# Kernel optimization log

Measured on AMD Instinct MI355X. Metric: run time of the kernel, lower is better.

## Reference

```python
import jax, jax.numpy as jnp
import numpy as np

V, E, H = 50000, 256, 512
BS, SEQ = 64, 200


def setup_inputs() -> dict:
    key = jax.random.key(0)
    ks = jax.random.split(key, 16)
    s = 0.05
    return {
        "input_idx": jax.random.randint(ks[0], (BS,), 0, V),
        "encoded": jax.random.normal(ks[1], (BS, SEQ, 2 * H), jnp.float32),
        "encoded_idx": jax.random.randint(ks[2], (BS, SEQ), 0, V),
        "prev_state": jax.random.normal(ks[3], (BS, H), jnp.float32),
        "weighted": jax.random.normal(ks[4], (BS, 1, 2 * H), jnp.float32),
        "order": 1,
        "embed_W": jax.random.normal(ks[5], (V, E), jnp.float32) * s,
        "Wih": jax.random.normal(ks[6], (3 * H, E + 2 * H), jnp.float32) * s,
        "Whh": jax.random.normal(ks[7], (3 * H, H), jnp.float32) * s,
        "bih": jax.random.normal(ks[8], (3 * H,), jnp.float32) * s,
        "bhh": jax.random.normal(ks[9], (3 * H,), jnp.float32) * s,
        "Ws_W": jax.random.normal(ks[10], (H, 2 * H), jnp.float32) * s,
        "Ws_b": jax.random.normal(ks[11], (H,), jnp.float32) * s,
        "Wo_W": jax.random.normal(ks[12], (V, H), jnp.float32) * s,
        "Wo_b": jax.random.normal(ks[13], (V,), jnp.float32) * s,
        "Wc_W": jax.random.normal(ks[14], (H, 2 * H), jnp.float32) * s,
        "Wc_b": jax.random.normal(ks[15], (H,), jnp.float32) * s,
    }


def reference(input_idx, encoded, encoded_idx, prev_state, weighted, order,
              embed_W, Wih, Whh, bih, bhh, Ws_W, Ws_b, Wo_W, Wo_b, Wc_W, Wc_b):
    bs, seq, _ = encoded.shape
    hidden = Ws_W.shape[0]
    vocab = Wo_W.shape[0]

    if order == 0:
        prev_state = encoded[:, 1] @ Ws_W.T + Ws_b            # [bs, H]
        weighted = jnp.zeros((bs, 1, 2 * hidden), encoded.dtype)

    # GRU single step (batch_first, seq len 1)
    x = jnp.concatenate([embed_W[input_idx], weighted[:, 0, :]], axis=1)  # [bs, E+2H]
    gi = x @ Wih.T + bih                                       # [bs, 3H]
    gh = prev_state @ Whh.T + bhh                              # [bs, 3H]
    i_r, i_z, i_n = jnp.split(gi, 3, axis=1)
    h_r, h_z, h_n = jnp.split(gh, 3, axis=1)
    r = jax.nn.sigmoid(i_r + h_r)
    z = jax.nn.sigmoid(i_z + h_z)
    n = jnp.tanh(i_n + r * h_n)
    state = (1.0 - z) * n + z * prev_state                     # [bs, H]

    # generate and copy scores
    score_g = state @ Wo_W.T + Wo_b                            # [bs, V]
    sc = jnp.tanh(encoded @ Wc_W.T + Wc_b)                     # [bs, seq, H]
    score_c = jnp.einsum('bsh,bh->bs', sc, state)              # [bs, seq]
    enc_mask = jnp.where(encoded_idx == 0, -1000.0, 0.0).astype(score_c.dtype)
    score_c = jnp.tanh(score_c + enc_mask)

    probs = jax.nn.softmax(jnp.concatenate([score_g, score_c], axis=1), axis=1)
    prob_g = probs[:, :vocab]                                  # [bs, V]
    prob_c = probs[:, vocab:]                                  # [bs, seq]

    # scatter-add copy probs into vocab slots
    prob_c_to_g = jnp.zeros((bs, vocab), probs.dtype).at[
        jnp.arange(bs)[:, None], encoded_idx].add(prob_c)
    out = (prob_g + prob_c_to_g)[:, None, :]                   # [bs, 1, V]

    # selective-read attention over positions matching input token
    m = (encoded_idx == input_idx[:, None]).astype(encoded.dtype)  # [bs, seq]
    ssum = m.sum(axis=1, keepdims=True)
    m = jnp.where(ssum > 1, m / ssum, m)
    attn = (prob_c * m)[:, None, :]                            # [bs, 1, seq]
    weighted_out = attn @ encoded                              # [bs, 1, 2H]

    return out, state, weighted_out
```

## Files before the change

### kernel.cpp

```cpp
#include <hip/hip_runtime.h>

#define V 50000
#define E_DIM 256
#define H_DIM 512
#define H2 1024
#define G3 1536
#define BSZ 64
#define SEQ 200
#define KX 1280
#define MROWS 12800
#define NBLK_WO 782

#define XBF_OFF   0
#define H0_OFF    40960
#define H0BF_OFF  73728
#define GI_OFF    90112
#define GH_OFF    188416
#define STBF_OFF  286720
#define WCBF_OFF  303104
#define SC_OFF    565248
#define REDG_OFF  616448
#define RED_OFF   716544
#define ENCBF_OFF 716672

#define OUT_STATE 3200000
#define OUT_W     3232768

typedef __attribute__((ext_vector_type(8))) short bf16x8;
typedef __attribute__((ext_vector_type(4))) float f32x4;

__device__ __forceinline__ float sigmf(float x) { return 1.f / (1.f + __expf(-x)); }

__device__ __forceinline__ ushort f2bf(float f) {
  uint u = __float_as_uint(f);
  uint r = (u + 0x7FFFu + ((u >> 16) & 1u)) >> 16;
  return (ushort)r;
}

__device__ __forceinline__ float tanhfast(float x) {
  float xc = fminf(15.f, fmaxf(-15.f, x));
  float e = __expf(2.f * xc);
  return (e - 1.f) * __builtin_amdgcn_rcpf(e + 1.f);
}

__device__ __forceinline__ bf16x8 cvt8(float4 a, float4 b) {
  union { bf16x8 v; uint u[4]; } r;
  asm("v_cvt_pk_bf16_f32 %0, %1, %2" : "=v"(r.u[0]) : "v"(a.x), "v"(a.y));
  asm("v_cvt_pk_bf16_f32 %0, %1, %2" : "=v"(r.u[1]) : "v"(a.z), "v"(a.w));
  asm("v_cvt_pk_bf16_f32 %0, %1, %2" : "=v"(r.u[2]) : "v"(b.x), "v"(b.y));
  asm("v_cvt_pk_bf16_f32 %0, %1, %2" : "=v"(r.u[3]) : "v"(b.z), "v"(b.w));
  return r.v;
}

__device__ __forceinline__ void gload16(const void* g, void* l) {
  __builtin_amdgcn_global_load_lds(
      (__attribute__((address_space(1))) void*)(g),
      (__attribute__((address_space(3))) void*)(l), 16, 0, 0);
}

__global__ void kprep(const float* __restrict__ Wc_W, ushort* __restrict__ Wc_bf,
                      const float* __restrict__ encoded, ushort* __restrict__ enc_bf,
                      const int* __restrict__ input_idx,
                      const float* __restrict__ prev_state, const float* __restrict__ weighted,
                      const int* __restrict__ order_p, const float* __restrict__ embed_W,
                      const float* __restrict__ Ws_W, const float* __restrict__ Ws_b,
                      ushort* __restrict__ x_bf, float* __restrict__ h0,
                      ushort* __restrict__ h0_bf) {
  int bid = blockIdx.x, tid = threadIdx.x;
  if (bid < 512) {
    int i = bid * 256 + tid;
    float4 v = ((const float4*)Wc_W)[i];
    ushort4 o;
    o.x = f2bf(v.x); o.y = f2bf(v.y); o.z = f2bf(v.z); o.w = f2bf(v.w);
    ((ushort4*)Wc_bf)[i] = o;
    return;
  }
  if (bid < 3712) {
    int base = (bid - 512) * 1024;
#pragma unroll
    for (int j = 0; j < 4; ++j) {
      int i = base + j * 256 + tid;
      float4 v = ((const float4*)encoded)[i];
      ushort4 o;
      o.x = f2bf(v.x); o.y = f2bf(v.y); o.z = f2bf(v.z); o.w = f2bf(v.w);
      ((ushort4*)enc_bf)[i] = o;
    }
    return;
  }
  int b = bid - 3712;
  int order = order_p[0];
  int idx = input_idx[b];
  x_bf[b * KX + tid] = f2bf(embed_W[(size_t)idx * E_DIM + tid]);
  if (order != 0) {
    for (int j = tid; j < H2; j += 256) x_bf[b * KX + E_DIM + j] = f2bf(weighted[b * H2 + j]);
    for (int j = tid; j < H_DIM; j += 256) {
      float v = prev_state[b * H_DIM + j];
      h0[b * H_DIM + j] = v;
      h0_bf[b * H_DIM + j] = f2bf(v);
    }
  } else {
    for (int j = tid; j < H2; j += 256) x_bf[b * KX + E_DIM + j] = 0;
    const float* er = encoded + ((size_t)b * SEQ + 1) * H2;
    for (int j = tid; j < H_DIM; j += 256) {
      float acc = Ws_b[j];
      const float* wr = Ws_W + (size_t)j * H2;
      for (int k = 0; k < H2; ++k) acc = fmaf(er[k], wr[k], acc);
      h0[b * H_DIM + j] = acc;
      h0_bf[b * H_DIM + j] = f2bf(acc);
    }
  }
}

__device__ __forceinline__ void gemm_small(const ushort* __restrict__ Abf,
                                           const float* __restrict__ W,
                                           const float* __restrict__ bias,
                                           float* __restrict__ out, int N, int kdim,
                                           int bid) {
  int tid = threadIdx.x;
  int lane = tid & 63, wv = tid >> 6;
  int l15 = lane & 15, lg = lane >> 4;
  int n0 = (bid * 4 + wv) * 16;
  int col = n0 + l15;
  bool valid = col < N;
  int colc = valid ? col : N - 1;
  f32x4 acc[4];
#pragma unroll
  for (int mt = 0; mt < 4; ++mt) acc[mt] = (f32x4){0.f, 0.f, 0.f, 0.f};
  const float* wrow = W + (size_t)colc * kdim + lg * 8;
  const ushort* arow = Abf + (size_t)l15 * kdim + lg * 8;
#pragma unroll 4
  for (int k0 = 0; k0 < kdim; k0 += 32) {
    float4 w0 = *(const float4*)(wrow + k0);
    float4 w1 = *(const float4*)(wrow + k0 + 4);
    bf16x8 bf = cvt8(w0, w1);
#pragma unroll
    for (int mt = 0; mt < 4; ++mt) {
      bf16x8 af = *(const bf16x8*)(arow + (size_t)mt * 16 * kdim + k0);
      acc[mt] = __builtin_amdgcn_mfma_f32_16x16x32_bf16(af, bf, acc[mt], 0, 0, 0);
    }
  }
  float bv = bias[colc];
  if (valid) {
#pragma unroll
    for (int mt = 0; mt < 4; ++mt)
#pragma unroll
      for (int r = 0; r < 4; ++r)
        out[(size_t)(mt * 16 + lg * 4 + r) * N + col] = acc[mt][r] + bv;
  }
}

__global__ __launch_bounds__(256) void mfma_gates(const ushort* __restrict__ x_bf,
                                                  const float* __restrict__ Wih,
                                                  const float* __restrict__ bih,
                                                  const ushort* __restrict__ h0_bf,
                                                  const float* __restrict__ Whh,
                                                  const float* __restrict__ bhh,
                                                  float* __restrict__ gi, float* __restrict__ gh) {
  if (blockIdx.y == 0)
    gemm_small(x_bf, Wih, bih, gi, G3, KX, blockIdx.x);
  else
    gemm_small(h0_bf, Whh, bhh, gh, G3, H_DIM, blockIdx.x);
}

__global__ void k2_gru(const float* __restrict__ gi, const float* __restrict__ gh,
                       const float* __restrict__ h0, float* __restrict__ state_out,
                       ushort* __restrict__ state_bf) {
  int b = blockIdx.x, j = threadIdx.x;
  float ir = gi[b * G3 + j], iz = gi[b * G3 + H_DIM + j], inn = gi[b * G3 + 2 * H_DIM + j];
  float hr = gh[b * G3 + j], hz = gh[b * G3 + H_DIM + j], hn = gh[b * G3 + 2 * H_DIM + j];
  float r = sigmf(ir + hr);
  float z = sigmf(iz + hz);
  float n = tanhf(inn + r * hn);
  float st = (1.f - z) * n + z * h0[b * H_DIM + j];
  state_out[b * H_DIM + j] = st;
  state_bf[b * H_DIM + j] = f2bf(st);
}

__global__ __launch_bounds__(256) void wo_stage(const ushort* __restrict__ state_bf,
                                                const float* __restrict__ Wo_W,
                                                const float* __restrict__ Wo_b,
                                                float* __restrict__ out,
                                                float* __restrict__ redg) {
  __shared__ char ldsW[4][4][2048];
  __shared__ float sm[4][64], ss[4][64];
  int tid = threadIdx.x, lane = tid & 63, wv = tid >> 6;
  int l15 = lane & 15, lg = lane >> 4;
  int bid = blockIdx.x;
  int col0 = bid * 64 + wv * 16 + l15;
  bool v0ok = col0 < V;
  int cc0 = v0ok ? col0 : V - 1;
  const float* s0 = Wo_W + (size_t)cc0 * H_DIM + lg * 8;
  const ushort* aptr = state_bf + (size_t)l15 * H_DIM + lg * 8;

  f32x4 acc[4];
#pragma unroll
  for (int mt = 0; mt < 4; ++mt) acc[mt] = (f32x4){0.f, 0.f, 0.f, 0.f};

#define STGW(buf, it) do {                      \
    char* d_ = &ldsW[wv][buf][0];               \
    gload16(s0 + (it) * 32,     d_);            \
    gload16(s0 + (it) * 32 + 4, d_ + 1024);     \
  } while (0)

  STGW(0, 0); STGW(1, 1); STGW(2, 2);
  asm volatile("" ::: "memory");
#pragma unroll 1
  for (int it = 0; it < 16; ++it) {
    int cur = it & 3;
    bf16x8 af0 = *(const bf16x8*)(aptr + 0 * 16 * H_DIM + it * 32);
    bf16x8 af1 = *(const bf16x8*)(aptr + 1 * 16 * H_DIM + it * 32);
    bf16x8 af2 = *(const bf16x8*)(aptr + 2 * 16 * H_DIM + it * 32);
    bf16x8 af3 = *(const bf16x8*)(aptr + 3 * 16 * H_DIM + it * 32);
    if (it == 0) {
      STGW(3, 3);
      asm volatile("s_waitcnt vmcnt(10)" ::: "memory");
    } else if (it == 1) {
      STGW(0, 4);
      asm volatile("s_waitcnt vmcnt(14)" ::: "memory");
    } else if (it < 13) {
      STGW((it + 3) & 3, it + 3);
      asm volatile("s_waitcnt vmcnt(18)" ::: "memory");
    } else if (it == 13) {
      asm volatile("s_waitcnt vmcnt(16)" ::: "memory");
    } else if (it == 14) {
      asm volatile("s_waitcnt vmcnt(14)" ::: "memory");
    } else {
      asm volatile("s_waitcnt vmcnt(12)" ::: "memory");
    }
    const char* base = &ldsW[wv][cur][0];
    float4 w00 = *(const float4*)(base + lane * 16);
    float4 w01 = *(const float4*)(base + 1024 + lane * 16);
    bf16x8 wf0 = cvt8(w00, w01);
    acc[0] = __builtin_amdgcn_mfma_f32_16x16x32_bf16(af0, wf0, acc[0], 0, 0, 0);
    acc[1] = __builtin_amdgcn_mfma_f32_16x16x32_bf16(af1, wf0, acc[1], 0, 0, 0);
    acc[2] = __builtin_amdgcn_mfma_f32_16x16x32_bf16(af2, wf0, acc[2], 0, 0, 0);
    acc[3] = __builtin_amdgcn_mfma_f32_16x16x32_bf16(af3, wf0, acc[3], 0, 0, 0);
  }
#undef STGW

  float bv0 = Wo_b[cc0];
#pragma unroll
  for (int mt = 0; mt < 4; ++mt)
#pragma unroll
    for (int r = 0; r < 4; ++r) {
      size_t row = (size_t)(mt * 16 + lg * 4 + r) * V;
      if (v0ok) out[row + col0] = acc[mt][r] + bv0;
    }
#pragma unroll
  for (int mt = 0; mt < 4; ++mt)
#pragma unroll
    for (int r = 0; r < 4; ++r) {
      float a0 = v0ok ? acc[mt][r] + bv0 : -1e30f;
      float mx = a0;
#pragma unroll
      for (int off = 1; off < 16; off <<= 1) mx = fmaxf(mx, __shfl_xor(mx, off, 64));
      float e = v0ok ? __expf(a0 - mx) : 0.f;
#pragma unroll
      for (int off = 1; off < 16; off <<= 1) e += __shfl_xor(e, off, 64);
      if (l15 == 0) {
        sm[wv][mt * 16 + lg * 4 + r] = mx;
        ss[wv][mt * 16 + lg * 4 + r] = e;
      }
    }
  __syncthreads();
  if (tid < 64) {
    float M = -1e30f, S = 0.f;
#pragma unroll
    for (int w = 0; w < 4; ++w) {
      float m2 = sm[w][tid], s2 = ss[w][tid];
      float mn = fmaxf(M, m2);
      S = S * __expf(M - mn) + s2 * __expf(m2 - mn);
      M = mn;
    }
    redg[((size_t)tid * NBLK_WO + bid) * 2] = M;
    redg[((size_t)tid * NBLK_WO + bid) * 2 + 1] = S;
  }
}

__global__ __launch_bounds__(256) void k4_mfma9(const ushort* __restrict__ enc_bf,
                                                const ushort* __restrict__ Wc_bf,
                                                const float* __restrict__ Wc_b,
                                                const float* __restrict__ state,
                                                float* __restrict__ scpart) {
  __shared__ char lds[2][24576];
  __shared__ float sred[4][64];
  int tid = threadIdx.x, lane = tid & 63, wv = tid >> 6;
  int l15 = lane & 15, lg = lane >> 4;
  int bid = blockIdx.x;
  int mtile = bid >> 2, ntile = bid & 3;
  int m0 = mtile * 64, n0 = ntile * 128;

  const ushort* asrc = enc_bf + (size_t)(m0 + wv * 16 + l15) * H2 + lg * 8;
  const ushort* bsrc0 = Wc_bf + (size_t)(n0 + (wv * 2 + 0) * 16 + l15) * H2 + lg * 8;
  const ushort* bsrc1 = Wc_bf + (size_t)(n0 + (wv * 2 + 1) * 16 + l15) * H2 + lg * 8;

  f32x4 acc[4][2];
#pragma unroll
  for (int mf = 0; mf < 4; ++mf)
#pragma unroll
    for (int nf = 0; nf < 2; ++nf) acc[mf][nf] = (f32x4){0.f, 0.f, 0.f, 0.f};

#define STG(buf, it) do {                                              \
    char* d_ = &lds[buf][0];                                           \
    gload16(asrc + (it) * 64,       d_ + (wv * 2 + 0) * 1024);         \
    gload16(asrc + (it) * 64 + 32,  d_ + (wv * 2 + 1) * 1024);         \
    gload16(bsrc0 + (it) * 64,      d_ + 8192 + (wv * 4 + 0) * 1024);  \
    gload16(bsrc0 + (it) * 64 + 32, d_ + 8192 + (wv * 4 + 1) * 1024);  \
    gload16(bsrc1 + (it) * 64,      d_ + 8192 + (wv * 4 + 2) * 1024);  \
    gload16(bsrc1 + (it) * 64 + 32, d_ + 8192 + (wv * 4 + 3) * 1024);  \
  } while (0)

  STG(0, 0);
  __syncthreads();
#pragma unroll 1
  for (int it = 0; it < 16; ++it) {
    int cur = it & 1;
    if (it < 15) STG(cur ^ 1, it + 1);
    const char* base = &lds[cur][0];
#pragma unroll
    for (int ks = 0; ks < 2; ++ks) {
      bf16x8 b0 = *(const bf16x8*)(base + 8192 + (wv * 4 + ks) * 1024 + lane * 16);
      bf16x8 b1 = *(const bf16x8*)(base + 8192 + (wv * 4 + 2 + ks) * 1024 + lane * 16);
#pragma unroll
      for (int mf = 0; mf < 4; ++mf) {
        bf16x8 a = *(const bf16x8*)(base + (mf * 2 + ks) * 1024 + lane * 16);
        acc[mf][0] = __builtin_amdgcn_mfma_f32_16x16x32_bf16(a, b0, acc[mf][0], 0, 0, 0);
        acc[mf][1] = __builtin_amdgcn_mfma_f32_16x16x32_bf16(a, b1, acc[mf][1], 0, 0, 0);
      }
    }
    __syncthreads();
  }
#undef STG

  float pv[4][4];
#pragma unroll
  for (int mf = 0; mf < 4; ++mf)
#pragma unroll
    for (int r = 0; r < 4; ++r) pv[mf][r] = 0.f;
#pragma unroll
  for (int nfl = 0; nfl < 2; ++nfl) {
    int n = n0 + (wv * 2 + nfl) * 16 + l15;
    float bias = Wc_b[n];
#pragma unroll
    for (int mf = 0; mf < 4; ++mf) {
      int mrow = m0 + mf * 16 + lg * 4;
#pragma unroll
      for (int r = 0; r < 4; ++r) {
        int b = (mrow + r) / SEQ;
        pv[mf][r] += tanhfast(acc[mf][nfl][r] + bias) * state[b * H_DIM + n];
      }
    }
  }
#pragma unroll
  for (int off = 1; off < 16; off <<= 1)
#pragma unroll
    for (int mf = 0; mf < 4; ++mf)
#pragma unroll
      for (int r = 0; r < 4; ++r) pv[mf][r] += __shfl_xor(pv[mf][r], off, 64);
  if (l15 == 0) {
#pragma unroll
    for (int mf = 0; mf < 4; ++mf)
#pragma unroll
      for (int r = 0; r < 4; ++r) sred[wv][mf * 16 + lg * 4 + r] = pv[mf][r];
  }
  __syncthreads();
  if (tid < 64) {
    float s = sred[0][tid] + sred[1][tid] + sred[2][tid] + sred[3][tid];
    scpart[(size_t)ntile * MROWS + m0 + tid] = s;
  }
}

__global__ void kred(const float* __restrict__ redg, const float* __restrict__ scpart,
                     const int* __restrict__ eidx, float* __restrict__ red) {
  int b = blockIdx.x, tid = threadIdx.x;
  float m = -1e30f, s = 0.f;
  for (int i = tid; i < NBLK_WO; i += 256) {
    float m2 = redg[((size_t)b * NBLK_WO + i) * 2];
    float s2 = redg[((size_t)b * NBLK_WO + i) * 2 + 1];
    float mn = fmaxf(m, m2);
    s = s * __expf(m - mn) + s2 * __expf(m2 - mn);
    m = mn;
  }
  for (int i = tid; i < SEQ; i += 256) {
    int idx = b * SEQ + i;
    int ei = eidx[idx];
    float scv = scpart[idx] + scpart[MROWS + idx] + scpart[2 * MROWS + idx] +
                scpart[3 * MROWS + idx];
    float sc = tanhf(scv + (ei == 0 ? -1000.f : 0.f));
    float mn = fmaxf(m, sc);
    s = s * __expf(m - mn) + __expf(sc - mn);
    m = mn;
  }
  __shared__ float ms[256], ssh[256];
  ms[tid] = m; ssh[tid] = s;
  __syncthreads();
  for (int off = 128; off > 0; off >>= 1) {
    if (tid < off) {
      float m2 = ms[tid + off], s2 = ssh[tid + off];
      float mn = fmaxf(ms[tid], m2);
      ssh[tid] = ssh[tid] * __expf(ms[tid] - mn) + s2 * __expf(m2 - mn);
      ms[tid] = mn;
    }
    __syncthreads();
  }
  if (tid == 0) {
    red[b * 2] = ms[0];
    red[b * 2 + 1] = ssh[0];
  }
}

__global__ void k7_probs(float* __restrict__ sg, const float* __restrict__ red) {
  int i = blockIdx.x * 256 + threadIdx.x;
  int b = i / 12500;
  float mm = red[b * 2], rd = 1.f / red[b * 2 + 1];
  float4* p = (float4*)sg;
  float4 v = p[i];
  v.x = __expf(v.x - mm) * rd;
  v.y = __expf(v.y - mm) * rd;
  v.z = __expf(v.z - mm) * rd;
  v.w = __expf(v.w - mm) * rd;
  p[i] = v;
}

__global__ void k8_copy(const float* __restrict__ scpart, const int* __restrict__ eidx,
                        const int* __restrict__ input_idx, const float* __restrict__ red,
                        const float* __restrict__ encoded, float* __restrict__ out,
                        float* __restrict__ wout) {
  int b = blockIdx.x, tid = threadIdx.x;
  __shared__ float att_s[SEQ];
  __shared__ int cnt_s[256];
  float mm = red[b * 2], rd = 1.f / red[b * 2 + 1];
  int inp = input_idx[b];
  int cnt = 0;
  for (int s = tid; s < SEQ; s += 256) {
    int idx = b * SEQ + s;
    int ei = eidx[idx];
    float scv = scpart[idx] + scpart[MROWS + idx] + scpart[2 * MROWS + idx] +
                scpart[3 * MROWS + idx];
    float sc = tanhf(scv + (ei == 0 ? -1000.f : 0.f));
    float p = __expf(sc - mm) * rd;
    bool mt = (ei == inp);
    att_s[s] = mt ? p : 0.f;
    cnt += mt ? 1 : 0;
    atomicAdd(&out[(size_t)b * V + ei], p);
  }
  cnt_s[tid] = cnt;
  __syncthreads();
  for (int off = 128; off > 0; off >>= 1) {
    if (tid < off) cnt_s[tid] += cnt_s[tid + off];
    __syncthreads();
  }
  int c = cnt_s[0];
  float scale = (c > 1) ? 1.f / (float)c : 1.f;
  float w0 = 0, w1 = 0, w2 = 0, w3 = 0;
  for (int s = 0; s < SEQ; ++s) {
    float a = att_s[s];
    if (a != 0.f) {
      const float* er = encoded + ((size_t)b * SEQ + s) * H2;
      w0 += a * er[tid];
      w1 += a * er[tid + 256];
      w2 += a * er[tid + 512];
      w3 += a * er[tid + 768];
    }
  }
  wout[b * H2 + tid] = w0 * scale;
  wout[b * H2 + tid + 256] = w1 * scale;
  wout[b * H2 + tid + 512] = w2 * scale;
  wout[b * H2 + tid + 768] = w3 * scale;
}

extern "C" void kernel_launch(void* const* d_in, const int* in_sizes, int n_in,
                              void* d_out, int out_size, void* d_ws, size_t ws_size,
                              hipStream_t stream) {
  const int* input_idx = (const int*)d_in[0];
  const float* encoded = (const float*)d_in[1];
  const int* encoded_idx = (const int*)d_in[2];
  const float* prev_state = (const float*)d_in[3];
  const float* weighted = (const float*)d_in[4];
  const int* order_p = (const int*)d_in[5];
  const float* embed_W = (const float*)d_in[6];
  const float* Wih = (const float*)d_in[7];
  const float* Whh = (const float*)d_in[8];
  const float* bih = (const float*)d_in[9];
  const float* bhh = (const float*)d_in[10];
  const float* Ws_W = (const float*)d_in[11];
  const float* Ws_b = (const float*)d_in[12];
  const float* Wo_W = (const float*)d_in[13];
  const float* Wo_b = (const float*)d_in[14];
  const float* Wc_W = (const float*)d_in[15];
  const float* Wc_b = (const float*)d_in[16];

  float* ws = (float*)d_ws;
  float* out = (float*)d_out;
  ushort* x_bf = (ushort*)(ws + XBF_OFF);
  float* h0 = ws + H0_OFF;
  ushort* h0_bf = (ushort*)(ws + H0BF_OFF);
  float* gi = ws + GI_OFF;
  float* gh = ws + GH_OFF;
  ushort* state_bf = (ushort*)(ws + STBF_OFF);
  ushort* Wc_bf = (ushort*)(ws + WCBF_OFF);
  float* scpart = ws + SC_OFF;
  float* redg = ws + REDG_OFF;
  float* red = ws + RED_OFF;
  ushort* enc_bf = (ushort*)(ws + ENCBF_OFF);
  float* state = out + OUT_STATE;
  float* wout = out + OUT_W;

  kprep<<<3776, 256, 0, stream>>>(Wc_W, Wc_bf, encoded, enc_bf, input_idx, prev_state,
                                  weighted, order_p, embed_W, Ws_W, Ws_b, x_bf, h0, h0_bf);
  mfma_gates<<<dim3(24, 2), 256, 0, stream>>>(x_bf, Wih, bih, h0_bf, Whh, bhh, gi, gh);
  k2_gru<<<64, 512, 0, stream>>>(gi, gh, h0, state, state_bf);
  wo_stage<<<NBLK_WO, 256, 0, stream>>>(state_bf, Wo_W, Wo_b, out, redg);
  k4_mfma9<<<800, 256, 0, stream>>>(enc_bf, Wc_bf, Wc_b, state, scpart);
  kred<<<64, 256, 0, stream>>>(redg, scpart, encoded_idx, red);
  k7_probs<<<3125, 256, 0, stream>>>(out, red);
  k8_copy<<<64, 256, 0, stream>>>(scpart, encoded_idx, input_idx, red, encoded, out, wout);
}
```

Measured before the change: 179.4 us.

## Split Wo projection across batch halves and stage state tile in LDS

Launches the output projection with a second grid dimension so each block handles 32 of the 64 batch rows, doubling the block count. The block's state rows are staged once into LDS instead of being re-read from global each iteration, and the weight prefetch shrinks from a 4-deep to a 2-deep buffer. Each Wo_W column tile, the dominant fp32 traffic, is now fetched by two blocks instead of one, in exchange for more parallelism and fewer accumulators per wave.

```diff
diff --git a/kernel.cpp b/kernel.cpp
--- a/kernel.cpp
+++ b/kernel.cpp
@@ -181,76 +181,69 @@
                                                 const float* __restrict__ Wo_b,
                                                 float* __restrict__ out,
                                                 float* __restrict__ redg) {
-  __shared__ char ldsW[4][4][2048];
-  __shared__ float sm[4][64], ss[4][64];
+  __shared__ char ldsA[32768];
+  __shared__ char ldsW[2][4][2048];
+  __shared__ float sm[4][32], ss[4][32];
   int tid = threadIdx.x, lane = tid & 63, wv = tid >> 6;
   int l15 = lane & 15, lg = lane >> 4;
-  int bid = blockIdx.x;
+  int bid = blockIdx.x, yh = blockIdx.y;
   int col0 = bid * 64 + wv * 16 + l15;
   bool v0ok = col0 < V;
   int cc0 = v0ok ? col0 : V - 1;
   const float* s0 = Wo_W + (size_t)cc0 * H_DIM + lg * 8;
-  const ushort* aptr = state_bf + (size_t)l15 * H_DIM + lg * 8;
-
-  f32x4 acc[4];
-#pragma unroll
-  for (int mt = 0; mt < 4; ++mt) acc[mt] = (f32x4){0.f, 0.f, 0.f, 0.f};
-
-#define STGW(buf, it) do {                      \
-    char* d_ = &ldsW[wv][buf][0];               \
-    gload16(s0 + (it) * 32,     d_);            \
-    gload16(s0 + (it) * 32 + 4, d_ + 1024);     \
-  } while (0)
-
-  STGW(0, 0); STGW(1, 1); STGW(2, 2);
-  asm volatile("" ::: "memory");
+
+#pragma unroll
+  for (int j = 0; j < 8; ++j) {
+    int slot = wv * 8 + j;
+    int mf = slot >> 4, it = slot & 15;
+    gload16(state_bf + (size_t)(yh * 32 + mf * 16 + l15) * H_DIM + it * 32 + lg * 8,
+            ldsA + slot * 1024);
+  }
+  {
+    char* d_ = &ldsW[0][wv][0];
+    gload16(s0, d_);
+    gload16(s0 + 4, d_ + 1024);
+  }
+  __syncthreads();
+
+  f32x4 acc[2];
+  acc[0] = (f32x4){0.f, 0.f, 0.f, 0.f};
+  acc[1] = (f32x4){0.f, 0.f, 0.f, 0.f};
+
 #pragma unroll 1
   for (int it = 0; it < 16; ++it) {
-    int cur = it & 3;
-    bf16x8 af0 = *(const bf16x8*)(aptr + 0 * 16 * H_DIM + it * 32);
-    bf16x8 af1 = *(const bf16x8*)(aptr + 1 * 16 * H_DIM + it * 32);
-    bf16x8 af2 = *(const bf16x8*)(aptr + 2 * 16 * H_DIM + it * 32);
-    bf16x8 af3 = *(const bf16x8*)(aptr + 3 * 16 * H_DIM + it * 32);
-    if (it == 0) {
-      STGW(3, 3);
-      asm volatile("s_waitcnt vmcnt(10)" ::: "memory");
-    } else if (it == 1) {
-      STGW(0, 4);
-      asm volatile("s_waitcnt vmcnt(14)" ::: "memory");
-    } else if (it < 13) {
-      STGW((it + 3) & 3, it + 3);
-      asm volatile("s_waitcnt vmcnt(18)" ::: "memory");
-    } else if (it == 13) {
-      asm volatile("s_waitcnt vmcnt(16)" ::: "memory");
-    } else if (it == 14) {
-      asm volatile("s_waitcnt vmcnt(14)" ::: "memory");
+    int cur = it & 1;
+    if (it < 15) {
+      char* d_ = &ldsW[cur ^ 1][wv][0];
+      gload16(s0 + (it + 1) * 32, d_);
+      gload16(s0 + (it + 1) * 32 + 4, d_ + 1024);
+      asm volatile("s_waitcnt vmcnt(2)" ::: "memory");
     } else {
-      asm volatile("s_waitcnt vmcnt(12)" ::: "memory");
-    }
-    const char* base = &ldsW[wv][cur][0];
-    float4 w00 = *(const float4*)(base + lane * 16);
-    float4 w01 = *(const float4*)(base + 1024 + lane * 16);
+      asm volatile("s_waitcnt vmcnt(0)" ::: "memory");
+    }
+    const char* wb = &ldsW[cur][wv][0];
+    float4 w00 = *(const float4*)(wb + lane * 16);
+    float4 w01 = *(const float4*)(wb + 1024 + lane * 16);
     bf16x8 wf0 = cvt8(w00, w01);
+    bf16x8 af0 = *(const bf16x8*)(ldsA + (0 * 16 + it) * 1024 + lane * 16);
+    bf16x8 af1 = *(const bf16x8*)(ldsA + (1 * 16 + it) * 1024 + lane * 16);
     acc[0] = __builtin_amdgcn_mfma_f32_16x16x32_bf16(af0, wf0, acc[0], 0, 0, 0);
     acc[1] = __builtin_amdgcn_mfma_f32_16x16x32_bf16(af1, wf0, acc[1], 0, 0, 0);
-    acc[2] = __builtin_amdgcn_mfma_f32_16x16x32_bf16(af2, wf0, acc[2], 0, 0, 0);
-    acc[3] = __builtin_amdgcn_mfma_f32_16x16x32_bf16(af3, wf0, acc[3], 0, 0, 0);
-  }
-#undef STGW
+  }
 
   float bv0 = Wo_b[cc0];
 #pragma unroll
-  for (int mt = 0; mt < 4; ++mt)
+  for (int mf = 0; mf < 2; ++mf)
 #pragma unroll
     for (int r = 0; r < 4; ++r) {
-      size_t row = (size_t)(mt * 16 + lg * 4 + r) * V;
-      if (v0ok) out[row + col0] = acc[mt][r] + bv0;
-    }
-#pragma unroll
-  for (int mt = 0; mt < 4; ++mt)
+      size_t row = (size_t)(yh * 32 + mf * 16 + lg * 4 + r) * V;
+      if (v0ok) out[row + col0] = acc[mf][r] + bv0;
+    }
+#pragma unroll
+  for (int mf = 0; mf < 2; ++mf)
 #pragma unroll
     for (int r = 0; r < 4; ++r) {
-      float a0 = v0ok ? acc[mt][r] + bv0 : -1e30f;
+      float a0 = v0ok ? acc[mf][r] + bv0 : -1e30f;
       float mx = a0;
 #pragma unroll
       for (int off = 1; off < 16; off <<= 1) mx = fmaxf(mx, __shfl_xor(mx, off, 64));
@@ -258,12 +251,12 @@
 #pragma unroll
       for (int off = 1; off < 16; off <<= 1) e += __shfl_xor(e, off, 64);
       if (l15 == 0) {
-        sm[wv][mt * 16 + lg * 4 + r] = mx;
-        ss[wv][mt * 16 + lg * 4 + r] = e;
+        sm[wv][mf * 16 + lg * 4 + r] = mx;
+        ss[wv][mf * 16 + lg * 4 + r] = e;
       }
     }
   __syncthreads();
-  if (tid < 64) {
+  if (tid < 32) {
     float M = -1e30f, S = 0.f;
 #pragma unroll
     for (int w = 0; w < 4; ++w) {
@@ -272,8 +265,8 @@
       S = S * __expf(M - mn) + s2 * __expf(m2 - mn);
       M = mn;
     }
-    redg[((size_t)tid * NBLK_WO + bid) * 2] = M;
-    redg[((size_t)tid * NBLK_WO + bid) * 2 + 1] = S;
+    redg[((size_t)(yh * 32 + tid) * NBLK_WO + bid) * 2] = M;
+    redg[((size_t)(yh * 32 + tid) * NBLK_WO + bid) * 2 + 1] = S;
   }
 }
 
@@ -510,7 +503,7 @@
                                   weighted, order_p, embed_W, Ws_W, Ws_b, x_bf, h0, h0_bf);
   mfma_gates<<<dim3(24, 2), 256, 0, stream>>>(x_bf, Wih, bih, h0_bf, Whh, bhh, gi, gh);
   k2_gru<<<64, 512, 0, stream>>>(gi, gh, h0, state, state_bf);
-  wo_stage<<<NBLK_WO, 256, 0, stream>>>(state_bf, Wo_W, Wo_b, out, redg);
+  wo_stage<<<dim3(NBLK_WO, 2), 256, 0, stream>>>(state_bf, Wo_W, Wo_b, out, redg);
   k4_mfma9<<<800, 256, 0, stream>>>(enc_bf, Wc_bf, Wc_b, state, scpart);
   kred<<<64, 256, 0, stream>>>(redg, scpart, encoded_idx, red);
   k7_probs<<<3125, 256, 0, stream>>>(out, red);
```

Result: no change. 180.6 us (+0.7%).
